# Kernel optimization log

Hardware: AMD Instinct MI355X
Metric: run time of the kernel (lower is better)

The kernel has to match this reference:

```python
import jax, jax.numpy as jnp
import numpy as np

EMB = 512       # emb_dim
H = 8           # n_heads
HD = EMB // H   # head_dim = 64
FREQ = 64       # freq_features
PERIOD = 0.1
N = 2048


def setup_inputs() -> dict:
    key = jax.random.key(0)
    ks = jax.random.split(key, 6)
    x = jax.random.normal(ks[0], (1, N, EMB), dtype=jnp.float32)
    v = jax.random.normal(ks[1], (1, N, 3), dtype=jnp.float32)
    vec_map = v / jnp.linalg.norm(v, axis=-1, keepdims=True)  # unit direction vectors
    s_in = 1.0 / np.sqrt(EMB)
    W_qkv = jax.random.normal(ks[2], (EMB, 3 * EMB), dtype=jnp.float32) * s_in
    b_qkv = jnp.zeros((3 * EMB,), dtype=jnp.float32)
    W_bias = jax.random.normal(ks[3], (FREQ, H), dtype=jnp.float32) * (1.0 / np.sqrt(FREQ))
    b_bias = jnp.zeros((H,), dtype=jnp.float32)
    W_out = jax.random.normal(ks[4], (EMB, EMB), dtype=jnp.float32) * s_in
    b_out = jnp.zeros((EMB,), dtype=jnp.float32)
    return {"x": x, "vec_map": vec_map, "W_qkv": W_qkv, "b_qkv": b_qkv,
            "W_bias": W_bias, "b_bias": b_bias, "W_out": W_out, "b_out": b_out}


def reference(x, vec_map, W_qkv, b_qkv, W_bias, b_bias, W_out, b_out):
    batch_dim = x.shape[:-2]
    n = x.shape[-2]
    # QKV projection -> (*, N, H, 3, HD)
    qkv = (x @ W_qkv + b_qkv).reshape(*batch_dim, n, H, 3, HD)
    q, k, v = (qkv[..., 0, :], qkv[..., 1, :], qkv[..., 2, :])
    # attention scores (*, Q, K, H), softmax over the K axis (axis=-2)
    attn = jnp.einsum('...qht,...kht->...qkh', q, k) / np.sqrt(HD)
    attn = jax.nn.softmax(attn, axis=-2)
    # relative bias from pairwise angles between direction vectors
    dot = jnp.einsum('...nc,...mc->...nm', vec_map, vec_map)
    angle = jnp.arccos(jnp.clip(dot, 0.0, 1.0)) / 0.001
    freqs = jnp.linspace(0.0, 1.0, FREQ // 2, dtype=jnp.float32) / PERIOD
    phase = freqs * angle[..., None]                      # (*, N, N, FREQ/2)
    pos = jnp.concatenate((jnp.sin(phase), jnp.cos(phase)), axis=-1)  # (*, N, N, FREQ)
    bias = pos @ W_bias + b_bias                          # (*, N, N, H)
    attn = attn + bias
    # weighted sum of values -> (*, N, EMB)
    y = jnp.einsum('...qkh,...kht->...qht', attn, v).reshape(*batch_dim, n, EMB)
    return y @ W_out + b_out
```

## Files before the change

### kernel.cpp

```cpp
#include <hip/hip_runtime.h>
#include <hip/hip_bf16.h>
#include <math.h>

#define NT 2048
#define EMBD 512
#define NH 8
#define QKV_LD 1536

typedef unsigned short u16;
typedef __attribute__((ext_vector_type(8))) short short8;
typedef __attribute__((ext_vector_type(4))) float v4f;

static __device__ __forceinline__ float bf2f(unsigned int u) {
    union { unsigned int i; float f; } c; c.i = u << 16; return c.f;
}
static __device__ __forceinline__ void unpack8(uint4 r, float* f) {
    f[0] = bf2f(r.x & 0xffffu); f[1] = bf2f(r.x >> 16);
    f[2] = bf2f(r.y & 0xffffu); f[3] = bf2f(r.y >> 16);
    f[4] = bf2f(r.z & 0xffffu); f[5] = bf2f(r.z >> 16);
    f[6] = bf2f(r.w & 0xffffu); f[7] = bf2f(r.w >> 16);
}
static __device__ __forceinline__ void unpack4(uint2 r, float* f) {
    f[0] = bf2f(r.x & 0xffffu); f[1] = bf2f(r.x >> 16);
    f[2] = bf2f(r.y & 0xffffu); f[3] = bf2f(r.y >> 16);
}
static __device__ __forceinline__ unsigned int f2bf(float x) {
    union { float f; unsigned int u; } c; c.f = x;
    return (c.u + 0x7fffu + ((c.u >> 16) & 1u)) >> 16;
}

__global__ __launch_bounds__(256) void gemm_qkv(const float* __restrict__ A,
    const float* __restrict__ B, const float* __restrict__ bias,
    u16* __restrict__ Cb, int M, int N, int K)
{
    __shared__ float As[16][68];
    __shared__ float Bs[16][68];
    const int n0 = blockIdx.x << 6, m0 = blockIdx.y << 6;
    const int t = threadIdx.x, tx = t & 15, ty = t >> 4;
    float acc[4][4] = {};
    for (int kb = 0; kb < K; kb += 16) {
#pragma unroll
        for (int l = 0; l < 4; ++l) {
            int e = t + (l << 8);
            int mm = e >> 4, kk = e & 15;
            As[kk][mm] = A[(size_t)(m0 + mm) * K + kb + kk];
        }
#pragma unroll
        for (int l = 0; l < 4; ++l) {
            int e = t + (l << 8);
            int kk = e >> 6, nn = e & 63;
            Bs[kk][nn] = B[(size_t)(kb + kk) * N + n0 + nn];
        }
        __syncthreads();
#pragma unroll
        for (int kk = 0; kk < 16; ++kk) {
            float a[4], b[4];
#pragma unroll
            for (int i = 0; i < 4; ++i) a[i] = As[kk][(ty << 2) + i];
#pragma unroll
            for (int j = 0; j < 4; ++j) b[j] = Bs[kk][(tx << 2) + j];
#pragma unroll
            for (int i = 0; i < 4; ++i)
#pragma unroll
                for (int j = 0; j < 4; ++j)
                    acc[i][j] = fmaf(a[i], b[j], acc[i][j]);
        }
        __syncthreads();
    }
#pragma unroll
    for (int i = 0; i < 4; ++i) {
        int m = m0 + (ty << 2) + i;
        unsigned int o[4];
#pragma unroll
        for (int j = 0; j < 4; ++j)
            o[j] = f2bf(acc[i][j] + bias[n0 + (tx << 2) + j]);
        uint2 w; w.x = o[0] | (o[1] << 16); w.y = o[2] | (o[3] << 16);
        *(uint2*)(Cb + (size_t)m * N + n0 + (tx << 2)) = w;
    }
}

__global__ __launch_bounds__(256) void transpose_v(const u16* __restrict__ qkvb,
                                                   u16* __restrict__ Vt)
{
    __shared__ u16 tile[64][72];
    const int h = blockIdx.y, k0 = blockIdx.x << 6;
    const int t = threadIdx.x;
    {
        int r = t >> 2, cg = (t & 3) << 4;
        const u16* src = qkvb + (size_t)(k0 + r) * QKV_LD + h * 192 + 128 + cg;
        *(uint4*)&tile[r][cg]     = *(const uint4*)src;
        *(uint4*)&tile[r][cg + 8] = *(const uint4*)(src + 8);
    }
    __syncthreads();
    {
        int c = t >> 2, kg = (t & 3) << 4;
        u16 tmp[16];
#pragma unroll
        for (int j = 0; j < 16; ++j) tmp[j] = tile[kg + j][c];
        u16* dst = Vt + ((size_t)h * 64 + c) * NT + k0 + kg;
        *(uint4*)dst       = *(uint4*)&tmp[0];
        *(uint4*)(dst + 8) = *(uint4*)&tmp[8];
    }
}

__global__ __launch_bounds__(256) void scores_mfma(const u16* __restrict__ qkvb,
                                                   u16* __restrict__ s)
{
    const int h = blockIdx.z;
    const int k0 = blockIdx.x << 7;
    const int q0 = (blockIdx.y << 7) + ((threadIdx.x >> 6) << 5);
    const int lane = threadIdx.x & 63;
    const int fr = lane & 15;
    const int kd = (lane >> 4) << 3;

    const u16* qbase = qkvb + (size_t)(q0 + fr) * QKV_LD + h * 192 + kd;
    const u16* kbase = qkvb + (size_t)(k0 + fr) * QKV_LD + h * 192 + 64 + kd;

    short8 aq[2][2];
    aq[0][0] = *(const short8*)(qbase);
    aq[0][1] = *(const short8*)(qbase + 32);
    aq[1][0] = *(const short8*)(qbase + (size_t)16 * QKV_LD);
    aq[1][1] = *(const short8*)(qbase + (size_t)16 * QKV_LD + 32);

    v4f acc[2][8] = {};
#pragma unroll
    for (int nt = 0; nt < 8; ++nt) {
        short8 b0 = *(const short8*)(kbase + (size_t)nt * 16 * QKV_LD);
        short8 b1 = *(const short8*)(kbase + (size_t)nt * 16 * QKV_LD + 32);
        acc[0][nt] = __builtin_amdgcn_mfma_f32_16x16x32_bf16(aq[0][0], b0, acc[0][nt], 0, 0, 0);
        acc[0][nt] = __builtin_amdgcn_mfma_f32_16x16x32_bf16(aq[0][1], b1, acc[0][nt], 0, 0, 0);
        acc[1][nt] = __builtin_amdgcn_mfma_f32_16x16x32_bf16(aq[1][0], b0, acc[1][nt], 0, 0, 0);
        acc[1][nt] = __builtin_amdgcn_mfma_f32_16x16x32_bf16(aq[1][1], b1, acc[1][nt], 0, 0, 0);
    }
    const int qr = (lane >> 4) << 2;
#pragma unroll
    for (int i = 0; i < 2; ++i)
#pragma unroll
        for (int nt = 0; nt < 8; ++nt)
#pragma unroll
            for (int r = 0; r < 4; ++r) {
                int q = q0 + (i << 4) + qr + r;
                int k = k0 + (nt << 4) + fr;
                s[((size_t)h * NT + q) * NT + k] = (u16)f2bf(acc[i][nt][r] * 0.125f);
            }
}

__global__ __launch_bounds__(256) void softmax_stats(const u16* __restrict__ s,
                                                     float* __restrict__ mOut,
                                                     float* __restrict__ izOut)
{
    const int row = blockIdx.x;
    const int t = threadIdx.x;
    const uint4 raw = *(const uint4*)(s + (size_t)row * NT + (t << 3));
    float v[8]; unpack8(raw, v);
    float m = v[0];
#pragma unroll
    for (int i = 1; i < 8; ++i) m = fmaxf(m, v[i]);
    __shared__ float red[256];
    red[t] = m; __syncthreads();
    for (int off = 128; off > 0; off >>= 1) {
        if (t < off) red[t] = fmaxf(red[t], red[t + off]);
        __syncthreads();
    }
    m = red[0];
    __syncthreads();
    float z = 0.f;
#pragma unroll
    for (int i = 0; i < 8; ++i) z += __expf(v[i] - m);
    red[t] = z; __syncthreads();
    for (int off = 128; off > 0; off >>= 1) {
        if (t < off) red[t] += red[t + off];
        __syncthreads();
    }
    if (t == 0) { mOut[row] = m; izOut[row] = 1.0f / red[0]; }
}

__global__ __launch_bounds__(256) void bias_kernel(u16* __restrict__ s,
    const float* __restrict__ vec, const float* __restrict__ Wb,
    const float* __restrict__ bb, const float* __restrict__ mbuf,
    const float* __restrict__ izbuf)
{
    __shared__ float wlds[64][8];
    __shared__ float flds[32];
    __shared__ float vql[96], vkl[96];
    __shared__ float bbl[8];
    __shared__ float bias_lds[8][32][33];

    const int t = threadIdx.x;
    int b = blockIdx.x, tq = 0, rem = 64;
    while (b >= rem) { b -= rem; ++tq; --rem; }
    const int tk = tq + b;
    const int q0 = tq << 5, k0 = tk << 5;

    for (int i = t; i < 512; i += 256) wlds[i >> 3][i & 7] = Wb[i];
    if (t < 32) flds[t] = __fdiv_rn(__fdiv_rn((float)t, 31.0f), 0.1f);
    if (t < 96) vql[t] = vec[q0 * 3 + t];
    else if (t < 192) vkl[t - 96] = vec[k0 * 3 + (t - 96)];
    else if (t < 200) bbl[t - 192] = bb[t - 192];
    __syncthreads();

    {
        const int qq = t & 31;
        const int kb = (t >> 5) << 2;
        const float a0 = vql[qq * 3], a1 = vql[qq * 3 + 1], a2 = vql[qq * 3 + 2];
        float ang[4];
#pragma unroll
        for (int j = 0; j < 4; ++j) {
            const int kk = kb + j;
            float c0 = vkl[kk * 3], c1 = vkl[kk * 3 + 1], c2 = vkl[kk * 3 + 2];
            float dot = __fadd_rn(__fadd_rn(__fmul_rn(a0, c0), __fmul_rn(a1, c1)),
                                  __fmul_rn(a2, c2));
            float dotc = fminf(fmaxf(dot, 0.0f), 1.0f);
            ang[j] = __fdiv_rn(acosf(dotc), 0.001f);
        }
        float bacc[4][8] = {};
#pragma unroll 4
        for (int i = 0; i < 32; ++i) {
            float ws[8], wc[8];
#pragma unroll
            for (int h = 0; h < 8; ++h) { ws[h] = wlds[i][h]; wc[h] = wlds[i + 32][h]; }
            const float fi = flds[i];
#pragma unroll
            for (int j = 0; j < 4; ++j) {
                float ph = __fmul_rn(fi, ang[j]);
                float rv = ph * 0.15915494309189535f;
                float rf = rv - floorf(rv);
                float si = __builtin_amdgcn_sinf(rf);
                float ci = __builtin_amdgcn_cosf(rf);
#pragma unroll
                for (int h = 0; h < 8; ++h) {
                    bacc[j][h] = fmaf(si, ws[h], bacc[j][h]);
                    bacc[j][h] = fmaf(ci, wc[h], bacc[j][h]);
                }
            }
        }
#pragma unroll
        for (int j = 0; j < 4; ++j)
#pragma unroll
            for (int h = 0; h < 8; ++h)
                bias_lds[h][qq][kb + j] = bacc[j][h];
    }
    __syncthreads();

    const int r = t >> 3;
    const int cg = (t & 7) << 2;
    {
        const int q = q0 + r;
#pragma unroll
        for (int h = 0; h < 8; ++h) {
            const float m = mbuf[h * NT + q], iz = izbuf[h * NT + q], bv = bbl[h];
            const size_t base = ((size_t)h * NT + q) * NT + k0 + cg;
            uint2 raw = *(const uint2*)(s + base);
            float v[4]; unpack4(raw, v);
            unsigned int o[4];
#pragma unroll
            for (int j = 0; j < 4; ++j) {
                float val = __expf(v[j] - m) * iz + bias_lds[h][r][cg + j] + bv;
                o[j] = f2bf(val);
            }
            uint2 w; w.x = o[0] | (o[1] << 16); w.y = o[2] | (o[3] << 16);
            *(uint2*)(s + base) = w;
        }
    }
    if (tk != tq) {
        const int q = k0 + r;
#pragma unroll
        for (int h = 0; h < 8; ++h) {
            const float m = mbuf[h * NT + q], iz = izbuf[h * NT + q], bv = bbl[h];
            const size_t base = ((size_t)h * NT + q) * NT + q0 + cg;
            uint2 raw = *(const uint2*)(s + base);
            float v[4]; unpack4(raw, v);
            unsigned int o[4];
#pragma unroll
            for (int j = 0; j < 4; ++j) {
                float val = __expf(v[j] - m) * iz + bias_lds[h][cg + j][r] + bv;
                o[j] = f2bf(val);
            }
            uint2 w; w.x = o[0] | (o[1] << 16); w.y = o[2] | (o[3] << 16);
            *(uint2*)(s + base) = w;
        }
    }
}

__global__ __launch_bounds__(256) void attnv_mfma(const u16* __restrict__ attn,
    const u16* __restrict__ Vt, float* __restrict__ ypart)
{
    const int h = blockIdx.y, z = blockIdx.z;
    const int q0 = (blockIdx.x << 6) + ((threadIdx.x >> 6) << 4);
    const int lane = threadIdx.x & 63;
    const int fr = lane & 15;
    const int kd = (lane >> 4) << 3;
    const int kbase = z << 9;

    const u16* arow  = attn + (size_t)(h * NT + q0 + fr) * NT + kbase + kd;
    const u16* vbase = Vt + ((size_t)h * 64 + fr) * NT + kbase + kd;

    v4f c[4] = {};
    for (int ks = 0; ks < 512; ks += 32) {
        short8 a = *(const short8*)(arow + ks);
#pragma unroll
        for (int nt = 0; nt < 4; ++nt) {
            short8 b = *(const short8*)(vbase + (size_t)nt * 16 * NT + ks);
            c[nt] = __builtin_amdgcn_mfma_f32_16x16x32_bf16(a, b, c[nt], 0, 0, 0);
        }
    }
    float* yp = ypart + (size_t)z * NT * EMBD;
    const int qr = (lane >> 4) << 2;
#pragma unroll
    for (int nt = 0; nt < 4; ++nt)
#pragma unroll
        for (int r = 0; r < 4; ++r)
            yp[(size_t)(q0 + qr + r) * EMBD + (h << 6) + (nt << 4) + fr] = c[nt][r];
}

__global__ __launch_bounds__(256) void gemm_f32_part(const float* __restrict__ A,
    const float* __restrict__ B, float* __restrict__ Cpart,
    int M, int N, int KS)
{
    __shared__ float As[16][68];
    __shared__ float Bs[16][68];
    const int n0 = blockIdx.x << 6, m0 = blockIdx.y << 6;
    const int kstart = blockIdx.z * KS;
    const int K = 512;
    const int t = threadIdx.x, tx = t & 15, ty = t >> 4;
    float acc[4][4] = {};
    for (int kb = kstart; kb < kstart + KS; kb += 16) {
#pragma unroll
        for (int l = 0; l < 4; ++l) {
            int e = t + (l << 8);
            int mm = e >> 4, kk = e & 15;
            As[kk][mm] = A[(size_t)(m0 + mm) * K + kb + kk];
        }
#pragma unroll
        for (int l = 0; l < 4; ++l) {
            int e = t + (l << 8);
            int kk = e >> 6, nn = e & 63;
            Bs[kk][nn] = B[(size_t)(kb + kk) * N + n0 + nn];
        }
        __syncthreads();
#pragma unroll
        for (int kk = 0; kk < 16; ++kk) {
            float a[4], b[4];
#pragma unroll
            for (int i = 0; i < 4; ++i) a[i] = As[kk][(ty << 2) + i];
#pragma unroll
            for (int j = 0; j < 4; ++j) b[j] = Bs[kk][(tx << 2) + j];
#pragma unroll
            for (int i = 0; i < 4; ++i)
#pragma unroll
                for (int j = 0; j < 4; ++j)
                    acc[i][j] = fmaf(a[i], b[j], acc[i][j]);
        }
        __syncthreads();
    }
    float* Cz = Cpart + (size_t)blockIdx.z * M * N;
#pragma unroll
    for (int i = 0; i < 4; ++i) {
        int m = m0 + (ty << 2) + i;
#pragma unroll
        for (int j = 0; j < 4; ++j) {
            int n = n0 + (tx << 2) + j;
            Cz[(size_t)m * N + n] = acc[i][j];
        }
    }
}

__global__ __launch_bounds__(256) void reduce_add(float* __restrict__ out,
    const float* __restrict__ parts, const float* __restrict__ bias,
    int nsplit, int MN, int N)
{
    int i = (blockIdx.x * 256 + threadIdx.x) << 2;
    if (i >= MN) return;
    float4 acc = *(const float4*)(parts + i);
    for (int sp = 1; sp < nsplit; ++sp) {
        float4 p = *(const float4*)(parts + (size_t)sp * MN + i);
        acc.x += p.x; acc.y += p.y; acc.z += p.z; acc.w += p.w;
    }
    if (bias) {
        float4 b = *(const float4*)(bias + (i & (N - 1)));
        acc.x += b.x; acc.y += b.y; acc.z += b.z; acc.w += b.w;
    }
    *(float4*)(out + i) = acc;
}

extern "C" void kernel_launch(void* const* d_in, const int* in_sizes, int n_in,
                              void* d_out, int out_size, void* d_ws, size_t ws_size,
                              hipStream_t stream)
{
    const float* x    = (const float*)d_in[0];
    const float* vec  = (const float*)d_in[1];
    const float* Wqkv = (const float*)d_in[2];
    const float* bqkv = (const float*)d_in[3];
    const float* Wb   = (const float*)d_in[4];
    const float* bb   = (const float*)d_in[5];
    const float* Wout = (const float*)d_in[6];
    const float* bout = (const float*)d_in[7];
    float* out = (float*)d_out;

    char* ws = (char*)d_ws;
    u16*   qkvb  = (u16*)(ws);
    u16*   sbuf  = (u16*)(ws + 6291456);
    u16*   Vt    = (u16*)(ws + 73400320);
    float* mbuf  = (float*)(ws + 75497472);
    float* izb   = (float*)(ws + 75563008);
    float* ybuf  = (float*)(ws + 75628544);
    float* parts = (float*)(ws + 79822848);

    gemm_qkv<<<dim3(24, 32), 256, 0, stream>>>(x, Wqkv, bqkv, qkvb, NT, QKV_LD, EMBD);
    transpose_v<<<dim3(32, 8), 256, 0, stream>>>(qkvb, Vt);
    scores_mfma<<<dim3(16, 16, 8), 256, 0, stream>>>(qkvb, sbuf);
    softmax_stats<<<NT * NH, 256, 0, stream>>>(sbuf, mbuf, izb);
    bias_kernel<<<2080, 256, 0, stream>>>(sbuf, vec, Wb, bb, mbuf, izb);
    attnv_mfma<<<dim3(32, 8, 4), 256, 0, stream>>>(sbuf, Vt, parts);
    reduce_add<<<1024, 256, 0, stream>>>(ybuf, parts, nullptr, 4, NT * EMBD, EMBD);
    gemm_f32_part<<<dim3(8, 32, 4), 256, 0, stream>>>(ybuf, Wout, parts, NT, EMBD, 128);
    reduce_add<<<1024, 256, 0, stream>>>(out, parts, bout, 4, NT * EMBD, EMBD);
}
```

Baseline: 297.0 us.

## Move QKV projection and positional-bias projection onto bf16 MFMA

The fp32 SIMT QKV GEMM is replaced by three kernels. Two of them split x and the transposed W_qkv into bf16 hi/lo pairs, and the third runs a split-bf16 MFMA GEMM (hi*hi + hi*lo + lo*hi) to approximate fp32 accuracy. In the bias kernel, the 64-feature by 8-head projection of the sin/cos features moves from per-thread FMA loops to MFMA. The angles and the projected bias are staged through LDS in the new layout. This adds preprocessing kernels, extra workspace traffic and scattered 2-byte stores in the GEMM epilogue, and the bias projection now rounds its inputs to bf16.

```diff
diff --git a/kernel.cpp b/kernel.cpp
--- a/kernel.cpp
+++ b/kernel.cpp
@@ -29,54 +29,103 @@
     return (c.u + 0x7fffu + ((c.u >> 16) & 1u)) >> 16;
 }
 
-__global__ __launch_bounds__(256) void gemm_qkv(const float* __restrict__ A,
-    const float* __restrict__ B, const float* __restrict__ bias,
-    u16* __restrict__ Cb, int M, int N, int K)
-{
-    __shared__ float As[16][68];
-    __shared__ float Bs[16][68];
+__global__ __launch_bounds__(256) void split_x(const float* __restrict__ x,
+    u16* __restrict__ xh, u16* __restrict__ xl)
+{
+    int i = (blockIdx.x * 256 + threadIdx.x) << 2;
+    float4 v = *(const float4*)(x + i);
+    float f[4] = {v.x, v.y, v.z, v.w};
+    unsigned int hi[4], lo[4];
+#pragma unroll
+    for (int j = 0; j < 4; ++j) {
+        hi[j] = f2bf(f[j]);
+        lo[j] = f2bf(f[j] - bf2f(hi[j]));
+    }
+    uint2 wh; wh.x = hi[0] | (hi[1] << 16); wh.y = hi[2] | (hi[3] << 16);
+    uint2 wl; wl.x = lo[0] | (lo[1] << 16); wl.y = lo[2] | (lo[3] << 16);
+    *(uint2*)(xh + i) = wh;
+    *(uint2*)(xl + i) = wl;
+}
+
+__global__ __launch_bounds__(256) void split_wt(const float* __restrict__ W,
+    u16* __restrict__ wth, u16* __restrict__ wtl)
+{
+    __shared__ float tile[64][65];
+    const int n0 = blockIdx.x << 6, k0 = blockIdx.y << 6;
+    const int t = threadIdx.x;
+    const int r = t >> 2, c4 = (t & 3) << 4;
+#pragma unroll
+    for (int j = 0; j < 4; ++j)
+        *(float4*)&tile[r][c4 + (j << 2)] =
+            *(const float4*)(W + (size_t)(k0 + r) * QKV_LD + n0 + c4 + (j << 2));
+    __syncthreads();
+    const int n_l = t >> 2;
+    u16 th[16], tl[16];
+#pragma unroll
+    for (int j = 0; j < 16; ++j) {
+        float f = tile[c4 + j][n_l];
+        unsigned int h = f2bf(f);
+        th[j] = (u16)h;
+        tl[j] = (u16)f2bf(f - bf2f(h));
+    }
+    u16* dh = wth + (size_t)(n0 + n_l) * EMBD + k0 + c4;
+    u16* dl = wtl + (size_t)(n0 + n_l) * EMBD + k0 + c4;
+    *(uint4*)dh       = *(uint4*)&th[0];
+    *(uint4*)(dh + 8) = *(uint4*)&th[8];
+    *(uint4*)dl       = *(uint4*)&tl[0];
+    *(uint4*)(dl + 8) = *(uint4*)&tl[8];
+}
+
+__global__ __launch_bounds__(256) void gemm_qkv_mfma(const u16* __restrict__ xh,
+    const u16* __restrict__ xl, const u16* __restrict__ wth,
+    const u16* __restrict__ wtl, const float* __restrict__ bias,
+    u16* __restrict__ qkvb)
+{
     const int n0 = blockIdx.x << 6, m0 = blockIdx.y << 6;
-    const int t = threadIdx.x, tx = t & 15, ty = t >> 4;
-    float acc[4][4] = {};
-    for (int kb = 0; kb < K; kb += 16) {
-#pragma unroll
-        for (int l = 0; l < 4; ++l) {
-            int e = t + (l << 8);
-            int mm = e >> 4, kk = e & 15;
-            As[kk][mm] = A[(size_t)(m0 + mm) * K + kb + kk];
-        }
-#pragma unroll
-        for (int l = 0; l < 4; ++l) {
-            int e = t + (l << 8);
-            int kk = e >> 6, nn = e & 63;
-            Bs[kk][nn] = B[(size_t)(kb + kk) * N + n0 + nn];
-        }
-        __syncthreads();
-#pragma unroll
-        for (int kk = 0; kk < 16; ++kk) {
-            float a[4], b[4];
-#pragma unroll
-            for (int i = 0; i < 4; ++i) a[i] = As[kk][(ty << 2) + i];
-#pragma unroll
-            for (int j = 0; j < 4; ++j) b[j] = Bs[kk][(tx << 2) + j];
-#pragma unroll
-            for (int i = 0; i < 4; ++i)
-#pragma unroll
-                for (int j = 0; j < 4; ++j)
-                    acc[i][j] = fmaf(a[i], b[j], acc[i][j]);
-        }
-        __syncthreads();
-    }
-#pragma unroll
-    for (int i = 0; i < 4; ++i) {
-        int m = m0 + (ty << 2) + i;
-        unsigned int o[4];
-#pragma unroll
-        for (int j = 0; j < 4; ++j)
-            o[j] = f2bf(acc[i][j] + bias[n0 + (tx << 2) + j]);
-        uint2 w; w.x = o[0] | (o[1] << 16); w.y = o[2] | (o[3] << 16);
-        *(uint2*)(Cb + (size_t)m * N + n0 + (tx << 2)) = w;
-    }
+    const int w = threadIdx.x >> 6, lane = threadIdx.x & 63;
+    const int wm = w >> 1, wn = w & 1;
+    const int fr = lane & 15, kd = (lane >> 4) << 3;
+
+    const u16* ah0 = xh + (size_t)(m0 + wm * 32 + fr) * EMBD + kd;
+    const u16* al0 = xl + (size_t)(m0 + wm * 32 + fr) * EMBD + kd;
+    const u16* bh0 = wth + (size_t)(n0 + wn * 32 + fr) * EMBD + kd;
+    const u16* bl0 = wtl + (size_t)(n0 + wn * 32 + fr) * EMBD + kd;
+
+    v4f acc[2][2] = {};
+    for (int kc = 0; kc < EMBD; kc += 32) {
+        short8 a_h[2], a_l[2], b_h[2], b_l[2];
+#pragma unroll
+        for (int im = 0; im < 2; ++im) {
+            a_h[im] = *(const short8*)(ah0 + (size_t)im * 16 * EMBD + kc);
+            a_l[im] = *(const short8*)(al0 + (size_t)im * 16 * EMBD + kc);
+        }
+#pragma unroll
+        for (int in = 0; in < 2; ++in) {
+            b_h[in] = *(const short8*)(bh0 + (size_t)in * 16 * EMBD + kc);
+            b_l[in] = *(const short8*)(bl0 + (size_t)in * 16 * EMBD + kc);
+        }
+#pragma unroll
+        for (int im = 0; im < 2; ++im)
+#pragma unroll
+            for (int in = 0; in < 2; ++in) {
+                acc[im][in] = __builtin_amdgcn_mfma_f32_16x16x32_bf16(a_h[im], b_h[in], acc[im][in], 0, 0, 0);
+                acc[im][in] = __builtin_amdgcn_mfma_f32_16x16x32_bf16(a_h[im], b_l[in], acc[im][in], 0, 0, 0);
+                acc[im][in] = __builtin_amdgcn_mfma_f32_16x16x32_bf16(a_l[im], b_h[in], acc[im][in], 0, 0, 0);
+            }
+    }
+    const int qr = (lane >> 4) << 2;
+#pragma unroll
+    for (int im = 0; im < 2; ++im)
+#pragma unroll
+        for (int in = 0; in < 2; ++in) {
+            int n = n0 + wn * 32 + in * 16 + fr;
+            float bv = bias[n];
+#pragma unroll
+            for (int r = 0; r < 4; ++r) {
+                int m = m0 + wm * 32 + im * 16 + qr + r;
+                qkvb[(size_t)m * QKV_LD + n] = (u16)f2bf(acc[im][in][r] + bv);
+            }
+        }
 }
 
 __global__ __launch_bounds__(256) void transpose_v(const u16* __restrict__ qkvb,
@@ -180,11 +229,11 @@
     const float* __restrict__ bb, const float* __restrict__ mbuf,
     const float* __restrict__ izbuf)
 {
-    __shared__ float wlds[64][8];
     __shared__ float flds[32];
     __shared__ float vql[96], vkl[96];
     __shared__ float bbl[8];
-    __shared__ float bias_lds[8][32][33];
+    __shared__ float ang_lds[1024];
+    __shared__ float bias_lds[1024][8];
 
     const int t = threadIdx.x;
     int b = blockIdx.x, tq = 0, rem = 64;
@@ -192,18 +241,15 @@
     const int tk = tq + b;
     const int q0 = tq << 5, k0 = tk << 5;
 
-    for (int i = t; i < 512; i += 256) wlds[i >> 3][i & 7] = Wb[i];
     if (t < 32) flds[t] = __fdiv_rn(__fdiv_rn((float)t, 31.0f), 0.1f);
-    if (t < 96) vql[t] = vec[q0 * 3 + t];
-    else if (t < 192) vkl[t - 96] = vec[k0 * 3 + (t - 96)];
-    else if (t < 200) bbl[t - 192] = bb[t - 192];
+    else if (t >= 32 && t < 128) vql[t - 32] = vec[q0 * 3 + (t - 32)];
+    else if (t < 224) vkl[t - 128] = vec[k0 * 3 + (t - 128)];
+    else if (t < 232) bbl[t - 224] = bb[t - 224];
     __syncthreads();
 
     {
-        const int qq = t & 31;
-        const int kb = (t >> 5) << 2;
+        const int qq = t & 31, kb = (t >> 5) << 2;
         const float a0 = vql[qq * 3], a1 = vql[qq * 3 + 1], a2 = vql[qq * 3 + 2];
-        float ang[4];
 #pragma unroll
         for (int j = 0; j < 4; ++j) {
             const int kk = kb + j;
@@ -211,34 +257,41 @@
             float dot = __fadd_rn(__fadd_rn(__fmul_rn(a0, c0), __fmul_rn(a1, c1)),
                                   __fmul_rn(a2, c2));
             float dotc = fminf(fmaxf(dot, 0.0f), 1.0f);
-            ang[j] = __fdiv_rn(acosf(dotc), 0.001f);
-        }
-        float bacc[4][8] = {};
-#pragma unroll 4
-        for (int i = 0; i < 32; ++i) {
-            float ws[8], wc[8];
-#pragma unroll
-            for (int h = 0; h < 8; ++h) { ws[h] = wlds[i][h]; wc[h] = wlds[i + 32][h]; }
-            const float fi = flds[i];
-#pragma unroll
-            for (int j = 0; j < 4; ++j) {
-                float ph = __fmul_rn(fi, ang[j]);
+            ang_lds[(qq << 5) + kk] = __fdiv_rn(acosf(dotc), 0.001f);
+        }
+    }
+    __syncthreads();
+
+    {
+        const int w = t >> 6, lane = t & 63;
+        const int fr = lane & 15, kd = (lane >> 4) << 3, qr = (lane >> 4) << 2;
+        short8 BS, BC;
+#pragma unroll
+        for (int j = 0; j < 8; ++j) {
+            float ws = (fr < 8) ? Wb[(kd + j) * 8 + fr] : 0.0f;
+            float wc = (fr < 8) ? Wb[(32 + kd + j) * 8 + fr] : 0.0f;
+            BS[j] = (short)f2bf(ws);
+            BC[j] = (short)f2bf(wc);
+        }
+        for (int tt = w; tt < 64; tt += 4) {
+            float ang = ang_lds[(tt << 4) + fr];
+            short8 AS, AC;
+#pragma unroll
+            for (int j = 0; j < 8; ++j) {
+                float ph = __fmul_rn(flds[kd + j], ang);
                 float rv = ph * 0.15915494309189535f;
                 float rf = rv - floorf(rv);
-                float si = __builtin_amdgcn_sinf(rf);
-                float ci = __builtin_amdgcn_cosf(rf);
-#pragma unroll
-                for (int h = 0; h < 8; ++h) {
-                    bacc[j][h] = fmaf(si, ws[h], bacc[j][h]);
-                    bacc[j][h] = fmaf(ci, wc[h], bacc[j][h]);
-                }
-            }
-        }
-#pragma unroll
-        for (int j = 0; j < 4; ++j)
-#pragma unroll
-            for (int h = 0; h < 8; ++h)
-                bias_lds[h][qq][kb + j] = bacc[j][h];
+                AS[j] = (short)f2bf(__builtin_amdgcn_sinf(rf));
+                AC[j] = (short)f2bf(__builtin_amdgcn_cosf(rf));
+            }
+            v4f c = {};
+            c = __builtin_amdgcn_mfma_f32_16x16x32_bf16(AS, BS, c, 0, 0, 0);
+            c = __builtin_amdgcn_mfma_f32_16x16x32_bf16(AC, BC, c, 0, 0, 0);
+            if (fr < 8)
+#pragma unroll
+                for (int r = 0; r < 4; ++r)
+                    bias_lds[(tt << 4) + qr + r][fr] = c[r];
+        }
     }
     __syncthreads();
 
@@ -255,11 +308,11 @@
             unsigned int o[4];
 #pragma unroll
             for (int j = 0; j < 4; ++j) {
-                float val = __expf(v[j] - m) * iz + bias_lds[h][r][cg + j] + bv;
+                float val = __expf(v[j] - m) * iz + bias_lds[(r << 5) + cg + j][h] + bv;
                 o[j] = f2bf(val);
             }
-            uint2 w; w.x = o[0] | (o[1] << 16); w.y = o[2] | (o[3] << 16);
-            *(uint2*)(s + base) = w;
+            uint2 wv; wv.x = o[0] | (o[1] << 16); wv.y = o[2] | (o[3] << 16);
+            *(uint2*)(s + base) = wv;
         }
     }
     if (tk != tq) {
@@ -273,11 +326,11 @@
             unsigned int o[4];
 #pragma unroll
             for (int j = 0; j < 4; ++j) {
-                float val = __expf(v[j] - m) * iz + bias_lds[h][cg + j][r] + bv;
+                float val = __expf(v[j] - m) * iz + bias_lds[((cg + j) << 5) + r][h] + bv;
                 o[j] = f2bf(val);
             }
-            uint2 w; w.x = o[0] | (o[1] << 16); w.y = o[2] | (o[3] << 16);
-            *(uint2*)(s + base) = w;
+            uint2 wv; wv.x = o[0] | (o[1] << 16); wv.y = o[2] | (o[3] << 16);
+            *(uint2*)(s + base) = wv;
         }
     }
 }
@@ -300,8 +353,8 @@
         short8 a = *(const short8*)(arow + ks);
 #pragma unroll
         for (int nt = 0; nt < 4; ++nt) {
-            short8 b = *(const short8*)(vbase + (size_t)nt * 16 * NT + ks);
-            c[nt] = __builtin_amdgcn_mfma_f32_16x16x32_bf16(a, b, c[nt], 0, 0, 0);
+            short8 bv = *(const short8*)(vbase + (size_t)nt * 16 * NT + ks);
+            c[nt] = __builtin_amdgcn_mfma_f32_16x16x32_bf16(a, bv, c[nt], 0, 0, 0);
         }
     }
     float* yp = ypart + (size_t)z * NT * EMBD;
@@ -340,16 +393,16 @@
         __syncthreads();
 #pragma unroll
         for (int kk = 0; kk < 16; ++kk) {
-            float a[4], b[4];
+            float a[4], bvv[4];
 #pragma unroll
             for (int i = 0; i < 4; ++i) a[i] = As[kk][(ty << 2) + i];
 #pragma unroll
-            for (int j = 0; j < 4; ++j) b[j] = Bs[kk][(tx << 2) + j];
+            for (int j = 0; j < 4; ++j) bvv[j] = Bs[kk][(tx << 2) + j];
 #pragma unroll
             for (int i = 0; i < 4; ++i)
 #pragma unroll
                 for (int j = 0; j < 4; ++j)
-                    acc[i][j] = fmaf(a[i], b[j], acc[i][j]);
+                    acc[i][j] = fmaf(a[i], bvv[j], acc[i][j]);
         }
         __syncthreads();
     }
@@ -405,8 +458,14 @@
     float* izb   = (float*)(ws + 75563008);
     float* ybuf  = (float*)(ws + 75628544);
     float* parts = (float*)(ws + 79822848);
-
-    gemm_qkv<<<dim3(24, 32), 256, 0, stream>>>(x, Wqkv, bqkv, qkvb, NT, QKV_LD, EMBD);
+    u16*   xh    = (u16*)(ws + 79822848);
+    u16*   xl    = (u16*)(ws + 81920000);
+    u16*   wth   = (u16*)(ws + 84017152);
+    u16*   wtl   = (u16*)(ws + 85590016);
+
+    split_x<<<1024, 256, 0, stream>>>(x, xh, xl);
+    split_wt<<<dim3(24, 8), 256, 0, stream>>>(Wqkv, wth, wtl);
+    gemm_qkv_mfma<<<dim3(24, 32), 256, 0, stream>>>(xh, xl, wth, wtl, bqkv, qkvb);
     transpose_v<<<dim3(32, 8), 256, 0, stream>>>(qkvb, Vt);
     scores_mfma<<<dim3(16, 16, 8), 256, 0, stream>>>(qkvb, sbuf);
     softmax_stats<<<NT * NH, 256, 0, stream>>>(sbuf, mbuf, izb);
```

Result: faster. 283.6 us (-4.5%).
